# Kernel optimization log

Hardware: AMD Instinct MI355X
Metric: run time of the kernel (lower is better)

Reference implementation:

```python
import jax, jax.numpy as jnp
import numpy as np

B, S, H, D = 4, 2048, 16, 64
DM = H * D  # model dim 1024


def _rope_sincos(seq_len, d2):
    # sin/cos tables for the rotated sub-dimension d2 (= head_dim // 2)
    inv_freq = 1.0 / (10000.0 ** (jnp.arange(0, d2, 2, dtype=jnp.float32) / d2))
    ang = jnp.arange(seq_len, dtype=jnp.float32)[:, None] * inv_freq[None, :]  # (S, d2/2)
    emb = jnp.concatenate([ang, ang], axis=-1)  # (S, d2)
    return jnp.sin(emb), jnp.cos(emb)


def _apply_rope(x, sin, cos):
    # x: (B, S, H, D). Only the first half of head_dim is rotated (faithful to
    # apply_rotary_pos_emb: split -> rotate x1 -> concat with untouched x2).
    x1, x2 = jnp.split(x, 2, axis=-1)  # each (B, S, H, D//2)
    a, b = jnp.split(x1, 2, axis=-1)
    rot = jnp.concatenate([-b, a], axis=-1)  # rotate_half(x1)
    sin = sin[None, :, None, :]
    cos = cos[None, :, None, :]
    return jnp.concatenate([x1 * cos + rot * sin, x2], axis=-1)


def setup_inputs() -> dict:
    key = jax.random.key(0)
    k1, k2 = jax.random.split(key)
    x = jax.random.normal(k1, (B, S, DM), dtype=jnp.float32)
    w_qkv = jax.random.normal(k2, (DM, 3 * H * D), dtype=jnp.float32) / np.sqrt(DM).astype(np.float32)
    mask = jnp.tril(jnp.ones((1, 1, S, S), dtype=bool))  # causal
    return {"x": x, "w_qkv": w_qkv, "mask": mask}


def reference(x, w_qkv, mask):
    b, s, _ = x.shape
    qkv = x @ w_qkv  # (B, S, 3*H*D) fused QKV projection (no bias)
    q, k, v = jnp.split(qkv, 3, axis=-1)
    q = q.reshape(b, s, H, D)
    k = k.reshape(b, s, H, D)
    v = v.reshape(b, s, H, D)
    sin, cos = _rope_sincos(s, D // 2)
    q = _apply_rope(q, sin, cos)
    k = _apply_rope(k, sin, cos)
    # full (B, H, S, S) score matrix, scaled by sqrt(head_dim)
    attn = jnp.einsum('bqhd,bkhd->bhqk', q, k) / jnp.sqrt(jnp.float32(D))
    attn = jnp.where(mask, attn, -jnp.inf)
    attn = jax.nn.softmax(attn, axis=-1)
    out = jnp.einsum('bhqk,bkhd->bqhd', attn, v)
    return out.reshape(b, s, H * D)
```

## Files before the change

### kernel.cpp

```cpp
#include <hip/hip_runtime.h>
#include <hip/hip_bf16.h>

#define SEQ 2048
#define DM 1024
#define NOUT 3072

typedef __attribute__((ext_vector_type(8))) short bf16x8;
typedef __attribute__((ext_vector_type(4))) float f32x4;
typedef __attribute__((ext_vector_type(16))) float f32x16;
typedef __attribute__((ext_vector_type(4))) unsigned int u32x4;

__device__ inline unsigned short bfb(float f) {
    __hip_bfloat16 h = __float2bfloat16(f);
    return __builtin_bit_cast(unsigned short, h);
}

__device__ inline unsigned pk2(float lo, float hi) {
    return (unsigned)bfb(lo) | ((unsigned)bfb(hi) << 16);
}

__device__ inline void gload_lds16(const void* g, void* l) {
    __builtin_amdgcn_global_load_lds(
        (const __attribute__((address_space(1))) unsigned int*)g,
        (__attribute__((address_space(3))) unsigned int*)l, 16, 0, 0);
}

#define M3(a, b, c) fmaxf(fmaxf((a), (b)), (c))

__global__ __launch_bounds__(256) void prep_kernel(
    const float* __restrict__ x, __hip_bfloat16* __restrict__ xb,
    const float* __restrict__ w, __hip_bfloat16* __restrict__ wT,
    float* __restrict__ sintab, float* __restrict__ costab) {
    __shared__ float t[64][65];
    const int b = blockIdx.x, tid = threadIdx.x;
    if (b < 8192) {
        int i = b * 256 + tid;
        float4 v = ((const float4*)x)[i];
        ushort4 o;
        o.x = bfb(v.x); o.y = bfb(v.y); o.z = bfb(v.z); o.w = bfb(v.w);
        ((ushort4*)xb)[i] = o;
    } else if (b < 8960) {
        const int idx = b - 8192;
        const int k0 = (idx & 15) * 64;
        const int n0 = (idx >> 4) * 64;
        for (int i = tid; i < 4096; i += 256) {
            int r = i >> 6, c = i & 63;
            t[r][c] = w[(size_t)(k0 + r) * NOUT + n0 + c];
        }
        __syncthreads();
        for (int i = tid; i < 4096; i += 256) {
            int nl = i >> 6, kl = i & 63;
            wT[(size_t)(n0 + nl) * DM + k0 + kl] = __float2bfloat16(t[kl][nl]);
        }
    } else {
        int i = (b - 8960) * 256 + tid;
        int f = i & 15, s = i >> 4;
        float inv = powf(10000.0f, -(float)f * (1.0f / 16.0f));
        float ang = (float)s * inv;
        sintab[i] = sinf(ang);
        costab[i] = cosf(ang);
    }
}

#define BM 128
#define BN 128
#define BK 32

__global__ __launch_bounds__(256) void qkv_gemm_kernel(
    const __hip_bfloat16* __restrict__ xb, const __hip_bfloat16* __restrict__ wT,
    const float* __restrict__ costab, const float* __restrict__ sintab,
    __hip_bfloat16* __restrict__ Qg, __hip_bfloat16* __restrict__ Kg,
    __hip_bfloat16* __restrict__ Vt) {
    __shared__ __hip_bfloat16 As[BM * BK];
    __shared__ __hip_bfloat16 Bs[BN * BK];
    const int tid = threadIdx.x, lane = tid & 63, wid = tid >> 6;
    const int wm = wid >> 1, wn = wid & 1;
    const int m0 = blockIdx.x * BM, n0 = blockIdx.y * BN;
    const int g = lane >> 4;

    f32x4 acc[4][4] = {};

    for (int k0 = 0; k0 < DM; k0 += BK) {
        __syncthreads();
#pragma unroll
        for (int c2 = 0; c2 < 2; ++c2) {
            const int chunk = wid * 2 + c2;
            gload_lds16(xb + (size_t)(m0 + chunk * 16 + (lane >> 2)) * DM + k0 + (lane & 3) * 8,
                        &As[chunk * 512]);
            gload_lds16(wT + (size_t)(n0 + chunk * 16 + (lane >> 2)) * DM + k0 + (lane & 3) * 8,
                        &Bs[chunk * 512]);
        }
        __syncthreads();
        bf16x8 a[4], b[4];
#pragma unroll
        for (int mf = 0; mf < 4; ++mf)
            a[mf] = *(const bf16x8*)&As[(wm * 64 + mf * 16 + (lane & 15)) * BK + (g << 3)];
#pragma unroll
        for (int nf = 0; nf < 4; ++nf)
            b[nf] = *(const bf16x8*)&Bs[(wn * 64 + nf * 16 + (lane & 15)) * BK + (g << 3)];
#pragma unroll
        for (int mf = 0; mf < 4; ++mf)
#pragma unroll
            for (int nf = 0; nf < 4; ++nf)
                acc[mf][nf] = __builtin_amdgcn_mfma_f32_16x16x32_bf16(a[mf], b[nf], acc[mf][nf], 0, 0, 0);
    }

    const int colbase = n0 + wn * 64;
    const int part = colbase >> 10;
    const int h = (colbase & 1023) >> 6;
    const int d0 = lane & 15;
    const int rowg0 = m0 + wm * 64 + (g << 2);

    if (part == 2) {
#pragma unroll
        for (int mf = 0; mf < 4; ++mf) {
            const int rbase = rowg0 + mf * 16;
            const int b = rbase >> 11, s = rbase & 2047;
            const size_t vb = (size_t)(b * 16 + h) * 64 * SEQ;
#pragma unroll
            for (int nf = 0; nf < 4; ++nf) {
                const int d = nf * 16 + d0;
                ushort4 pk;
                pk.x = bfb(acc[mf][nf][0]);
                pk.y = bfb(acc[mf][nf][1]);
                pk.z = bfb(acc[mf][nf][2]);
                pk.w = bfb(acc[mf][nf][3]);
                *(ushort4*)((unsigned short*)Vt + vb + (size_t)d * SEQ + s) = pk;
            }
        }
    } else {
        __hip_bfloat16* __restrict__ dstT = part ? Kg : Qg;
        const float sc = part ? 1.0f : 0.125f * 1.44269504088896340736f;
#pragma unroll
        for (int mf = 0; mf < 4; ++mf) {
#pragma unroll
            for (int j = 0; j < 4; ++j) {
                const int mg = rowg0 + mf * 16 + j;
                const int b = mg >> 11, s = mg & 2047;
                const float cv = costab[s * 16 + d0];
                const float sv = sintab[s * 16 + d0];
                const float v0 = acc[mf][0][j], v1 = acc[mf][1][j];
                __hip_bfloat16* dst = dstT + ((size_t)(b * 16 + h) * SEQ + s) * 64;
                dst[d0]      = __float2bfloat16((v0 * cv - v1 * sv) * sc);
                dst[16 + d0] = __float2bfloat16((v1 * cv + v0 * sv) * sc);
                dst[32 + d0] = __float2bfloat16(acc[mf][2][j] * sc);
                dst[48 + d0] = __float2bfloat16(acc[mf][3][j] * sc);
            }
        }
    }
}

__global__ __launch_bounds__(256) void attn_fwd_kernel(
    const __hip_bfloat16* __restrict__ Qg, const __hip_bfloat16* __restrict__ Kg,
    const __hip_bfloat16* __restrict__ Vt, float* __restrict__ out) {
    __shared__ __align__(16) char smem[2][16384];
    const int tid = threadIdx.x, lane = tid & 63, wid = tid >> 6;
    const int qt = 15 - (blockIdx.x >> 6);
    const int bh = blockIdx.x & 63;
    const size_t base = (size_t)bh << 17;
    const int ql = lane & 31, hi = lane >> 5;
    const int qb = (qt << 7) + (wid << 5);
    const int qrow = qb + ql;
    const int nkt = 2 * qt + 2;
    const unsigned short* Kgu = (const unsigned short*)Kg + base;
    const unsigned short* Vtu = (const unsigned short*)Vt + base;
    const int b = bh >> 4, h = bh & 15;
    const int lo16 = lane << 4;

    bf16x8 qfrag[4];
    {
        const unsigned short* qp = (const unsigned short*)Qg + base + (size_t)qrow * 64 + hi * 8;
#pragma unroll
        for (int c = 0; c < 4; ++c) qfrag[c] = *(const bf16x8*)(qp + c * 16);
    }

    f32x16 accO[2] = {};
    float m = -INFINITY, l = 0.0f;

    const unsigned short* stsrc;
    int stdst;
    if (wid < 2) {
        stsrc = Kgu + (size_t)(wid * 32 + ql) * 64 + hi * 8;
        stdst = wid * 4096;
    } else {
        stsrc = Vtu + (size_t)((wid - 2) * 32 + ql) * SEQ + hi * 8;
        stdst = 8192 + (wid - 2) * 4096;
    }

    {
#pragma unroll
        for (int c = 0; c < 4; ++c)
            gload_lds16(stsrc + c * 16, &smem[0][stdst + c * 1024]);
    }

    int cur = 0;
#pragma unroll 1
    for (int kt = 0; kt < nkt; ++kt) {
        const int k0 = kt << 6;
        if (kt + 1 < nkt) {
            const int kn = (kt + 1) << 6;
            const unsigned short* sn = (wid < 2) ? stsrc + (size_t)kn * 64 : stsrc + kn;
            char* nb = &smem[cur ^ 1][stdst];
#pragma unroll
            for (int c = 0; c < 4; ++c)
                gload_lds16(sn + c * 16, nb + c * 1024);
            asm volatile("s_waitcnt vmcnt(4)" ::: "memory");
        } else {
            asm volatile("s_waitcnt vmcnt(0)" ::: "memory");
        }
        __builtin_amdgcn_s_barrier();
        __builtin_amdgcn_sched_barrier(0);

        if (k0 <= qb + 31) {
            const char* Ks = smem[cur];
            const char* Vs = smem[cur] + 8192;

            f32x16 st[2] = {};
            __builtin_amdgcn_s_setprio(1);
#pragma unroll
            for (int c = 0; c < 4; ++c) {
                bf16x8 kf0 = *(const bf16x8*)(Ks + c * 1024 + lo16);
                bf16x8 kf1 = *(const bf16x8*)(Ks + 4096 + c * 1024 + lo16);
                st[0] = __builtin_amdgcn_mfma_f32_32x32x16_bf16(kf0, qfrag[c], st[0], 0, 0, 0);
                st[1] = __builtin_amdgcn_mfma_f32_32x32x16_bf16(kf1, qfrag[c], st[1], 0, 0, 0);
            }
            __builtin_amdgcn_s_setprio(0);

            if (k0 + 63 > qb) {
#pragma unroll
                for (int t = 0; t < 2; ++t)
#pragma unroll
                    for (int r = 0; r < 16; ++r) {
                        const int kg = k0 + 32 * t + (r & 3) + 8 * (r >> 2) + 4 * hi;
                        if (kg > qrow) st[t][r] = -INFINITY;
                    }
            }

            float x0 = M3(st[0][0], st[0][1], st[0][2]);
            float x1 = M3(st[0][3], st[0][4], st[0][5]);
            float x2 = M3(st[0][6], st[0][7], st[0][8]);
            float x3 = M3(st[0][9], st[0][10], st[0][11]);
            float x4 = M3(st[0][12], st[0][13], st[0][14]);
            float x5 = M3(st[0][15], st[1][0], st[1][1]);
            float x6 = M3(st[1][2], st[1][3], st[1][4]);
            float x7 = M3(st[1][5], st[1][6], st[1][7]);
            float x8 = M3(st[1][8], st[1][9], st[1][10]);
            float x9 = M3(st[1][11], st[1][12], st[1][13]);
            float xa = fmaxf(st[1][14], st[1][15]);
            float y0 = M3(x0, x1, x2), y1 = M3(x3, x4, x5);
            float y2 = M3(x6, x7, x8), y3 = M3(x9, xa, y0);
            float tm = M3(y1, y2, y3);
            tm = fmaxf(tm, __shfl_xor(tm, 32, 64));

            if (__any(tm > m + 8.0f)) {
                const float mn = fmaxf(m, tm);
                const float scl = __builtin_amdgcn_exp2f(m - mn);
                m = mn;
                l *= scl;
#pragma unroll
                for (int db = 0; db < 2; ++db)
#pragma unroll
                    for (int r = 0; r < 16; ++r) accO[db][r] *= scl;
            }

            float s0 = 0.0f, s1 = 0.0f, s2 = 0.0f, s3 = 0.0f;
#pragma unroll
            for (int r = 0; r < 16; r += 4) {
                float p00 = __builtin_amdgcn_exp2f(st[0][r + 0] - m);
                float p01 = __builtin_amdgcn_exp2f(st[0][r + 1] - m);
                float p02 = __builtin_amdgcn_exp2f(st[0][r + 2] - m);
                float p03 = __builtin_amdgcn_exp2f(st[0][r + 3] - m);
                float p10 = __builtin_amdgcn_exp2f(st[1][r + 0] - m);
                float p11 = __builtin_amdgcn_exp2f(st[1][r + 1] - m);
                float p12 = __builtin_amdgcn_exp2f(st[1][r + 2] - m);
                float p13 = __builtin_amdgcn_exp2f(st[1][r + 3] - m);
                st[0][r + 0] = p00; st[0][r + 1] = p01; st[0][r + 2] = p02; st[0][r + 3] = p03;
                st[1][r + 0] = p10; st[1][r + 1] = p11; st[1][r + 2] = p12; st[1][r + 3] = p13;
                s0 += p00 + p01; s1 += p02 + p03;
                s2 += p10 + p11; s3 += p12 + p13;
            }
            float ls = (s0 + s1) + (s2 + s3);
            ls += __shfl_xor(ls, 32, 64);
            l += ls;

            bf16x8 pfrag[4];
#pragma unroll
            for (int ks = 0; ks < 4; ++ks) {
                const int t = ks >> 1, rb = (ks & 1) * 8;
                unsigned a0 = pk2(st[t][rb + 0], st[t][rb + 1]);
                unsigned a1 = pk2(st[t][rb + 2], st[t][rb + 3]);
                unsigned b0 = pk2(st[t][rb + 4], st[t][rb + 5]);
                unsigned b1 = pk2(st[t][rb + 6], st[t][rb + 7]);
                asm("v_permlane32_swap_b32 %0, %1" : "+v"(a0), "+v"(b0));
                asm("v_permlane32_swap_b32 %0, %1" : "+v"(a1), "+v"(b1));
                u32x4 w;
                w[0] = a0;
                w[1] = a1;
                w[2] = b0;
                w[3] = b1;
                pfrag[ks] = __builtin_bit_cast(bf16x8, w);
            }

            __builtin_amdgcn_s_setprio(1);
#pragma unroll
            for (int ks = 0; ks < 4; ++ks) {
#pragma unroll
                for (int db = 0; db < 2; ++db) {
                    bf16x8 vf = *(const bf16x8*)(Vs + (db * 4 + ks) * 1024 + lo16);
                    accO[db] = __builtin_amdgcn_mfma_f32_32x32x16_bf16(vf, pfrag[ks], accO[db], 0, 0, 0);
                }
            }
            __builtin_amdgcn_s_setprio(0);
        }

        __builtin_amdgcn_sched_barrier(0);
        __builtin_amdgcn_s_barrier();
        cur ^= 1;
    }

    const float invl = 1.0f / l;
    float* orow = out + (size_t)(b * SEQ + qrow) * DM + h * 64;
#pragma unroll
    for (int db = 0; db < 2; ++db)
#pragma unroll
        for (int rg = 0; rg < 4; ++rg) {
            float4 v;
            v.x = accO[db][rg * 4 + 0] * invl;
            v.y = accO[db][rg * 4 + 1] * invl;
            v.z = accO[db][rg * 4 + 2] * invl;
            v.w = accO[db][rg * 4 + 3] * invl;
            *(float4*)(orow + db * 32 + rg * 8 + hi * 4) = v;
        }
}

extern "C" void kernel_launch(void* const* d_in, const int* in_sizes, int n_in,
                              void* d_out, int out_size, void* d_ws, size_t ws_size,
                              hipStream_t stream) {
    const float* x = (const float*)d_in[0];
    const float* w = (const float*)d_in[1];
    float* out = (float*)d_out;
    char* ws = (char*)d_ws;

    __hip_bfloat16* xb  = (__hip_bfloat16*)(ws + 0);
    __hip_bfloat16* wT  = (__hip_bfloat16*)(ws + 16777216);
    __hip_bfloat16* Qg  = (__hip_bfloat16*)(ws + 23068672);
    __hip_bfloat16* Kg  = (__hip_bfloat16*)(ws + 39845888);
    __hip_bfloat16* Vt  = (__hip_bfloat16*)(ws + 56623104);
    float* costab       = (float*)(ws + 73400320);
    float* sintab       = (float*)(ws + 73531392);

    prep_kernel<<<dim3(9088), dim3(256), 0, stream>>>(x, xb, w, wT, sintab, costab);
    qkv_gemm_kernel<<<dim3(64, 24), dim3(256), 0, stream>>>(xb, wT, costab, sintab, Qg, Kg, Vt);
    attn_fwd_kernel<<<dim3(1024), dim3(256), 0, stream>>>(Qg, Kg, Vt, out);
}
```

Measured before the change: 142.6 us.

## Enlarge QKV GEMM tiles to 256x256 with double-buffered LDS prefetch

Rewrites the QKV projection GEMM to use 512-thread blocks computing 256x256 output tiles with a K step of 64. A 128KB dynamic LDS buffer is double-buffered so the next K slab is loaded while MFMAs run on the current one. MFMA sections are wrapped in raised wave priority. Each wave now holds 8x4 accumulator fragments, which raises operand reuse and cuts per-tile sync overhead. In exchange, the grid shrinks to 384 blocks with about one block per CU, which may cause tail imbalance, and register pressure rises.

```diff
diff --git a/kernel.cpp b/kernel.cpp
--- a/kernel.cpp
+++ b/kernel.cpp
@@ -62,58 +62,86 @@
     }
 }
 
-#define BM 128
-#define BN 128
-#define BK 32
-
-__global__ __launch_bounds__(256) void qkv_gemm_kernel(
+__device__ __forceinline__ void qkv_tile(const char* Ab, const char* Bb, f32x4 (&acc)[8][4]) {
+#pragma unroll
+    for (int ks = 0; ks < 2; ++ks) {
+        bf16x8 a[8], b[4];
+#pragma unroll
+        for (int mf = 0; mf < 8; ++mf) a[mf] = *(const bf16x8*)(Ab + mf * 2048 + ks * 1024);
+#pragma unroll
+        for (int nf = 0; nf < 4; ++nf) b[nf] = *(const bf16x8*)(Bb + nf * 2048 + ks * 1024);
+        __builtin_amdgcn_s_setprio(1);
+#pragma unroll
+        for (int mf = 0; mf < 8; ++mf)
+#pragma unroll
+            for (int nf = 0; nf < 4; ++nf)
+                acc[mf][nf] = __builtin_amdgcn_mfma_f32_16x16x32_bf16(a[mf], b[nf], acc[mf][nf], 0, 0, 0);
+        __builtin_amdgcn_s_setprio(0);
+    }
+}
+
+__global__ __launch_bounds__(512, 2) void qkv_gemm_kernel(
     const __hip_bfloat16* __restrict__ xb, const __hip_bfloat16* __restrict__ wT,
     const float* __restrict__ costab, const float* __restrict__ sintab,
     __hip_bfloat16* __restrict__ Qg, __hip_bfloat16* __restrict__ Kg,
     __hip_bfloat16* __restrict__ Vt) {
-    __shared__ __hip_bfloat16 As[BM * BK];
-    __shared__ __hip_bfloat16 Bs[BN * BK];
+    extern __shared__ __align__(16) char smc[];
     const int tid = threadIdx.x, lane = tid & 63, wid = tid >> 6;
-    const int wm = wid >> 1, wn = wid & 1;
-    const int m0 = blockIdx.x * BM, n0 = blockIdx.y * BN;
-    const int g = lane >> 4;
-
-    f32x4 acc[4][4] = {};
-
-    for (int k0 = 0; k0 < DM; k0 += BK) {
+    const int wm = wid >> 2, wn = wid & 3;
+    const int m0 = blockIdx.x * 256, n0 = blockIdx.y * 256;
+
+    const int row_lane = lane >> 2;
+    const int k_lane = (lane & 3) * 8;
+    const __hip_bfloat16* sA0 = xb + (size_t)(m0 +       wid * 16 + row_lane) * DM + k_lane;
+    const __hip_bfloat16* sA1 = xb + (size_t)(m0 + 128 + wid * 16 + row_lane) * DM + k_lane;
+    const __hip_bfloat16* sB0 = wT + (size_t)(n0 +       wid * 16 + row_lane) * DM + k_lane;
+    const __hip_bfloat16* sB1 = wT + (size_t)(n0 + 128 + wid * 16 + row_lane) * DM + k_lane;
+    const int dA0 = wid * 2048, dA1 = 16384 + wid * 2048;
+    const int dB0 = 32768 + wid * 2048, dB1 = 49152 + wid * 2048;
+
+    const int fragoff = (lane & 15) * 64 + (lane >> 4) * 16;
+    const char* Abase = smc + wm * 16384 + fragoff;
+    const char* Bbase = smc + 32768 + (wn >> 1) * 16384 + (wn & 1) * 8192 + fragoff;
+
+    f32x4 acc[8][4] = {};
+
+#pragma unroll
+    for (int s = 0; s < 2; ++s) {
+        gload_lds16(sA0 + s * 32, smc + dA0 + s * 1024);
+        gload_lds16(sA1 + s * 32, smc + dA1 + s * 1024);
+        gload_lds16(sB0 + s * 32, smc + dB0 + s * 1024);
+        gload_lds16(sB1 + s * 32, smc + dB1 + s * 1024);
+    }
+    __syncthreads();
+
+#pragma unroll 1
+    for (int t = 0; t < 15; ++t) {
+        const int kk = (t + 1) * 64;
+        const int nb = ((t + 1) & 1) * 65536;
+#pragma unroll
+        for (int s = 0; s < 2; ++s) {
+            gload_lds16(sA0 + kk + s * 32, smc + nb + dA0 + s * 1024);
+            gload_lds16(sA1 + kk + s * 32, smc + nb + dA1 + s * 1024);
+            gload_lds16(sB0 + kk + s * 32, smc + nb + dB0 + s * 1024);
+            gload_lds16(sB1 + kk + s * 32, smc + nb + dB1 + s * 1024);
+        }
+        __builtin_amdgcn_sched_barrier(0);
+        const int cb = (t & 1) * 65536;
+        qkv_tile(Abase + cb, Bbase + cb, acc);
         __syncthreads();
-#pragma unroll
-        for (int c2 = 0; c2 < 2; ++c2) {
-            const int chunk = wid * 2 + c2;
-            gload_lds16(xb + (size_t)(m0 + chunk * 16 + (lane >> 2)) * DM + k0 + (lane & 3) * 8,
-                        &As[chunk * 512]);
-            gload_lds16(wT + (size_t)(n0 + chunk * 16 + (lane >> 2)) * DM + k0 + (lane & 3) * 8,
-                        &Bs[chunk * 512]);
-        }
-        __syncthreads();
-        bf16x8 a[4], b[4];
-#pragma unroll
-        for (int mf = 0; mf < 4; ++mf)
-            a[mf] = *(const bf16x8*)&As[(wm * 64 + mf * 16 + (lane & 15)) * BK + (g << 3)];
-#pragma unroll
-        for (int nf = 0; nf < 4; ++nf)
-            b[nf] = *(const bf16x8*)&Bs[(wn * 64 + nf * 16 + (lane & 15)) * BK + (g << 3)];
-#pragma unroll
-        for (int mf = 0; mf < 4; ++mf)
-#pragma unroll
-            for (int nf = 0; nf < 4; ++nf)
-                acc[mf][nf] = __builtin_amdgcn_mfma_f32_16x16x32_bf16(a[mf], b[nf], acc[mf][nf], 0, 0, 0);
-    }
+    }
+    qkv_tile(Abase + 65536, Bbase + 65536, acc);
 
     const int colbase = n0 + wn * 64;
     const int part = colbase >> 10;
     const int h = (colbase & 1023) >> 6;
     const int d0 = lane & 15;
-    const int rowg0 = m0 + wm * 64 + (g << 2);
+    const int g = lane >> 4;
+    const int rowg0 = m0 + wm * 128 + (g << 2);
 
     if (part == 2) {
 #pragma unroll
-        for (int mf = 0; mf < 4; ++mf) {
+        for (int mf = 0; mf < 8; ++mf) {
             const int rbase = rowg0 + mf * 16;
             const int b = rbase >> 11, s = rbase & 2047;
             const size_t vb = (size_t)(b * 16 + h) * 64 * SEQ;
@@ -132,7 +160,7 @@
         __hip_bfloat16* __restrict__ dstT = part ? Kg : Qg;
         const float sc = part ? 1.0f : 0.125f * 1.44269504088896340736f;
 #pragma unroll
-        for (int mf = 0; mf < 4; ++mf) {
+        for (int mf = 0; mf < 8; ++mf) {
 #pragma unroll
             for (int j = 0; j < 4; ++j) {
                 const int mg = rowg0 + mf * 16 + j;
@@ -349,7 +377,14 @@
     float* costab       = (float*)(ws + 73400320);
     float* sintab       = (float*)(ws + 73531392);
 
+    static bool qkv_attr_set = false;
+    if (!qkv_attr_set) {
+        hipFuncSetAttribute((const void*)qkv_gemm_kernel,
+                            hipFuncAttributeMaxDynamicSharedMemorySize, 131072);
+        qkv_attr_set = true;
+    }
+
     prep_kernel<<<dim3(9088), dim3(256), 0, stream>>>(x, xb, w, wT, sintab, costab);
-    qkv_gemm_kernel<<<dim3(64, 24), dim3(256), 0, stream>>>(xb, wT, costab, sintab, Qg, Kg, Vt);
+    qkv_gemm_kernel<<<dim3(32, 12), dim3(512), 131072, stream>>>(xb, wT, costab, sintab, Qg, Kg, Vt);
     attn_fwd_kernel<<<dim3(1024), dim3(256), 0, stream>>>(Qg, Kg, Vt, out);
 }
```

Result: slower. 148.5 us (+4.1%).

## Double-buffer QKV GEMM with larger 256x128 tiles and 512 threads

Applied to the files above, without the earlier changes.

Rewrites the QKV projection GEMM to use 256x128 block tiles with 8 waves, BK=64, and a double-buffered dynamic LDS pipeline. Loads for the next k-step are issued before computing the current one, with vmcnt-based waits and s_setprio around the MFMA bursts. The aim is to hide global-to-LDS latency and halve the number of barriers per unit of work. In exchange it uses 96KB of LDS and one block per CU, which lowers occupancy, and it halves the grid size.

```diff
diff --git a/kernel.cpp b/kernel.cpp
--- a/kernel.cpp
+++ b/kernel.cpp
@@ -62,53 +62,80 @@
     }
 }
 
-#define BM 128
-#define BN 128
-#define BK 32
-
-__global__ __launch_bounds__(256) void qkv_gemm_kernel(
+#define PERBUF 49152
+
+__device__ __forceinline__ void qkv_tile(const char* Ab, const char* Bb, f32x4 (&acc)[4][4]) {
+#pragma unroll
+    for (int ks = 0; ks < 2; ++ks) {
+        bf16x8 a[4], b[4];
+#pragma unroll
+        for (int mf = 0; mf < 4; ++mf) a[mf] = *(const bf16x8*)(Ab + mf * 2048 + ks * 1024);
+#pragma unroll
+        for (int nf = 0; nf < 4; ++nf) b[nf] = *(const bf16x8*)(Bb + nf * 2048 + ks * 1024);
+        __builtin_amdgcn_s_setprio(1);
+#pragma unroll
+        for (int mf = 0; mf < 4; ++mf)
+#pragma unroll
+            for (int nf = 0; nf < 4; ++nf)
+                acc[mf][nf] = __builtin_amdgcn_mfma_f32_16x16x32_bf16(a[mf], b[nf], acc[mf][nf], 0, 0, 0);
+        __builtin_amdgcn_s_setprio(0);
+    }
+}
+
+__global__ __launch_bounds__(512, 1) void qkv_gemm_kernel(
     const __hip_bfloat16* __restrict__ xb, const __hip_bfloat16* __restrict__ wT,
     const float* __restrict__ costab, const float* __restrict__ sintab,
     __hip_bfloat16* __restrict__ Qg, __hip_bfloat16* __restrict__ Kg,
     __hip_bfloat16* __restrict__ Vt) {
-    __shared__ __hip_bfloat16 As[BM * BK];
-    __shared__ __hip_bfloat16 Bs[BN * BK];
+    extern __shared__ __align__(16) char smc[];
     const int tid = threadIdx.x, lane = tid & 63, wid = tid >> 6;
     const int wm = wid >> 1, wn = wid & 1;
-    const int m0 = blockIdx.x * BM, n0 = blockIdx.y * BN;
-    const int g = lane >> 4;
+    const int m0 = blockIdx.x * 256, n0 = blockIdx.y * 128;
+    const int rl = lane & 15;
+    const int kl = (lane >> 4) * 8;
+
+    const __hip_bfloat16* sA = xb + (size_t)(m0 + wid * 32 + rl) * DM + kl;
+    const __hip_bfloat16* sB = wT + (size_t)(n0 + wid * 16 + rl) * DM + kl;
+
+#define QKV_STAGE(kk, bufoff)                                                           \
+    do {                                                                                \
+        _Pragma("unroll")                                                               \
+        for (int s = 0; s < 4; ++s)                                                     \
+            gload_lds16(sA + (size_t)(s >> 1) * (16 * DM) + (kk) + (s & 1) * 32,        \
+                        smc + (bufoff) + wid * 4096 + (s >> 1) * 2048 + (s & 1) * 1024);\
+        _Pragma("unroll")                                                               \
+        for (int s = 0; s < 2; ++s)                                                     \
+            gload_lds16(sB + (kk) + s * 32,                                             \
+                        smc + (bufoff) + 32768 + wid * 2048 + s * 1024);                \
+    } while (0)
 
     f32x4 acc[4][4] = {};
-
-    for (int k0 = 0; k0 < DM; k0 += BK) {
-        __syncthreads();
-#pragma unroll
-        for (int c2 = 0; c2 < 2; ++c2) {
-            const int chunk = wid * 2 + c2;
-            gload_lds16(xb + (size_t)(m0 + chunk * 16 + (lane >> 2)) * DM + k0 + (lane & 3) * 8,
-                        &As[chunk * 512]);
-            gload_lds16(wT + (size_t)(n0 + chunk * 16 + (lane >> 2)) * DM + k0 + (lane & 3) * 8,
-                        &Bs[chunk * 512]);
-        }
-        __syncthreads();
-        bf16x8 a[4], b[4];
-#pragma unroll
-        for (int mf = 0; mf < 4; ++mf)
-            a[mf] = *(const bf16x8*)&As[(wm * 64 + mf * 16 + (lane & 15)) * BK + (g << 3)];
-#pragma unroll
-        for (int nf = 0; nf < 4; ++nf)
-            b[nf] = *(const bf16x8*)&Bs[(wn * 64 + nf * 16 + (lane & 15)) * BK + (g << 3)];
-#pragma unroll
-        for (int mf = 0; mf < 4; ++mf)
-#pragma unroll
-            for (int nf = 0; nf < 4; ++nf)
-                acc[mf][nf] = __builtin_amdgcn_mfma_f32_16x16x32_bf16(a[mf], b[nf], acc[mf][nf], 0, 0, 0);
-    }
+    const int Aoff = wm * 8192 + lane * 16;
+    const int Boff = 32768 + wn * 8192 + lane * 16;
+
+    QKV_STAGE(0, 0);
+
+#pragma unroll 1
+    for (int t = 0; t < 15; ++t) {
+        const int kk = (t + 1) * 64;
+        QKV_STAGE(kk, ((t + 1) & 1) * PERBUF);
+        asm volatile("s_waitcnt vmcnt(6)" ::: "memory");
+        __builtin_amdgcn_s_barrier();
+        __builtin_amdgcn_sched_barrier(0);
+        const int cb = (t & 1) * PERBUF;
+        qkv_tile(smc + cb + Aoff, smc + cb + Boff, acc);
+        __builtin_amdgcn_sched_barrier(0);
+        __builtin_amdgcn_s_barrier();
+    }
+    asm volatile("s_waitcnt vmcnt(0)" ::: "memory");
+    __builtin_amdgcn_s_barrier();
+    qkv_tile(smc + PERBUF + Aoff, smc + PERBUF + Boff, acc);
 
     const int colbase = n0 + wn * 64;
     const int part = colbase >> 10;
     const int h = (colbase & 1023) >> 6;
     const int d0 = lane & 15;
+    const int g = lane >> 4;
     const int rowg0 = m0 + wm * 64 + (g << 2);
 
     if (part == 2) {
@@ -349,7 +376,14 @@
     float* costab       = (float*)(ws + 73400320);
     float* sintab       = (float*)(ws + 73531392);
 
+    static bool qkv_attr_set = false;
+    if (!qkv_attr_set) {
+        hipFuncSetAttribute((const void*)qkv_gemm_kernel,
+                            hipFuncAttributeMaxDynamicSharedMemorySize, 98304);
+        qkv_attr_set = true;
+    }
+
     prep_kernel<<<dim3(9088), dim3(256), 0, stream>>>(x, xb, w, wT, sintab, costab);
-    qkv_gemm_kernel<<<dim3(64, 24), dim3(256), 0, stream>>>(xb, wT, costab, sintab, Qg, Kg, Vt);
+    qkv_gemm_kernel<<<dim3(32, 24), dim3(512), 98304, stream>>>(xb, wT, costab, sintab, Qg, Kg, Vt);
     attn_fwd_kernel<<<dim3(1024), dim3(256), 0, stream>>>(Qg, Kg, Vt, out);
 }
```

After: 157.2 us. 1.1x slower.

## Load K/V fragments directly from global memory, dropping LDS staging and barriers

Applied to the files above, without the earlier changes.

The attention kernel no longer stages K and V tiles into double-buffered shared memory via global_load_lds with block-wide barriers. Each wave now reads its K and V MFMA fragments straight from global memory and runs only its own causal trip count (per-wave nkt). This removes LDS traffic, barriers and the idle iterations of waves already past the diagonal. The cost is that all four waves re-read the same K/V from global memory or L2 without any software prefetch, so load latency is exposed on every iteration.

```diff
diff --git a/kernel.cpp b/kernel.cpp
--- a/kernel.cpp
+++ b/kernel.cpp
@@ -153,7 +153,6 @@
 __global__ __launch_bounds__(256) void attn_fwd_kernel(
     const __hip_bfloat16* __restrict__ Qg, const __hip_bfloat16* __restrict__ Kg,
     const __hip_bfloat16* __restrict__ Vt, float* __restrict__ out) {
-    __shared__ __align__(16) char smem[2][16384];
     const int tid = threadIdx.x, lane = tid & 63, wid = tid >> 6;
     const int qt = 15 - (blockIdx.x >> 6);
     const int bh = blockIdx.x & 63;
@@ -161,11 +160,10 @@
     const int ql = lane & 31, hi = lane >> 5;
     const int qb = (qt << 7) + (wid << 5);
     const int qrow = qb + ql;
-    const int nkt = 2 * qt + 2;
-    const unsigned short* Kgu = (const unsigned short*)Kg + base;
-    const unsigned short* Vtu = (const unsigned short*)Vt + base;
     const int b = bh >> 4, h = bh & 15;
-    const int lo16 = lane << 4;
+
+    const unsigned short* kp = (const unsigned short*)Kg + base + (size_t)ql * 64 + hi * 8;
+    const unsigned short* vp = (const unsigned short*)Vt + base + (size_t)ql * SEQ + hi * 8;
 
     bf16x8 qfrag[4];
     {
@@ -177,145 +175,115 @@
     f32x16 accO[2] = {};
     float m = -INFINITY, l = 0.0f;
 
-    const unsigned short* stsrc;
-    int stdst;
-    if (wid < 2) {
-        stsrc = Kgu + (size_t)(wid * 32 + ql) * 64 + hi * 8;
-        stdst = wid * 4096;
-    } else {
-        stsrc = Vtu + (size_t)((wid - 2) * 32 + ql) * SEQ + hi * 8;
-        stdst = 8192 + (wid - 2) * 4096;
-    }
-
-    {
-#pragma unroll
-        for (int c = 0; c < 4; ++c)
-            gload_lds16(stsrc + c * 16, &smem[0][stdst + c * 1024]);
-    }
-
-    int cur = 0;
+    const int nkt = ((qb + 31) >> 6) + 1;
+
 #pragma unroll 1
     for (int kt = 0; kt < nkt; ++kt) {
         const int k0 = kt << 6;
-        if (kt + 1 < nkt) {
-            const int kn = (kt + 1) << 6;
-            const unsigned short* sn = (wid < 2) ? stsrc + (size_t)kn * 64 : stsrc + kn;
-            char* nb = &smem[cur ^ 1][stdst];
-#pragma unroll
-            for (int c = 0; c < 4; ++c)
-                gload_lds16(sn + c * 16, nb + c * 1024);
-            asm volatile("s_waitcnt vmcnt(4)" ::: "memory");
-        } else {
-            asm volatile("s_waitcnt vmcnt(0)" ::: "memory");
-        }
-        __builtin_amdgcn_s_barrier();
-        __builtin_amdgcn_sched_barrier(0);
-
-        if (k0 <= qb + 31) {
-            const char* Ks = smem[cur];
-            const char* Vs = smem[cur] + 8192;
-
-            f32x16 st[2] = {};
-            __builtin_amdgcn_s_setprio(1);
-#pragma unroll
-            for (int c = 0; c < 4; ++c) {
-                bf16x8 kf0 = *(const bf16x8*)(Ks + c * 1024 + lo16);
-                bf16x8 kf1 = *(const bf16x8*)(Ks + 4096 + c * 1024 + lo16);
-                st[0] = __builtin_amdgcn_mfma_f32_32x32x16_bf16(kf0, qfrag[c], st[0], 0, 0, 0);
-                st[1] = __builtin_amdgcn_mfma_f32_32x32x16_bf16(kf1, qfrag[c], st[1], 0, 0, 0);
-            }
-            __builtin_amdgcn_s_setprio(0);
-
-            if (k0 + 63 > qb) {
-#pragma unroll
-                for (int t = 0; t < 2; ++t)
-#pragma unroll
-                    for (int r = 0; r < 16; ++r) {
-                        const int kg = k0 + 32 * t + (r & 3) + 8 * (r >> 2) + 4 * hi;
-                        if (kg > qrow) st[t][r] = -INFINITY;
-                    }
-            }
-
-            float x0 = M3(st[0][0], st[0][1], st[0][2]);
-            float x1 = M3(st[0][3], st[0][4], st[0][5]);
-            float x2 = M3(st[0][6], st[0][7], st[0][8]);
-            float x3 = M3(st[0][9], st[0][10], st[0][11]);
-            float x4 = M3(st[0][12], st[0][13], st[0][14]);
-            float x5 = M3(st[0][15], st[1][0], st[1][1]);
-            float x6 = M3(st[1][2], st[1][3], st[1][4]);
-            float x7 = M3(st[1][5], st[1][6], st[1][7]);
-            float x8 = M3(st[1][8], st[1][9], st[1][10]);
-            float x9 = M3(st[1][11], st[1][12], st[1][13]);
-            float xa = fmaxf(st[1][14], st[1][15]);
-            float y0 = M3(x0, x1, x2), y1 = M3(x3, x4, x5);
-            float y2 = M3(x6, x7, x8), y3 = M3(x9, xa, y0);
-            float tm = M3(y1, y2, y3);
-            tm = fmaxf(tm, __shfl_xor(tm, 32, 64));
-
-            if (__any(tm > m + 8.0f)) {
-                const float mn = fmaxf(m, tm);
-                const float scl = __builtin_amdgcn_exp2f(m - mn);
-                m = mn;
-                l *= scl;
-#pragma unroll
-                for (int db = 0; db < 2; ++db)
-#pragma unroll
-                    for (int r = 0; r < 16; ++r) accO[db][r] *= scl;
-            }
-
-            float s0 = 0.0f, s1 = 0.0f, s2 = 0.0f, s3 = 0.0f;
-#pragma unroll
-            for (int r = 0; r < 16; r += 4) {
-                float p00 = __builtin_amdgcn_exp2f(st[0][r + 0] - m);
-                float p01 = __builtin_amdgcn_exp2f(st[0][r + 1] - m);
-                float p02 = __builtin_amdgcn_exp2f(st[0][r + 2] - m);
-                float p03 = __builtin_amdgcn_exp2f(st[0][r + 3] - m);
-                float p10 = __builtin_amdgcn_exp2f(st[1][r + 0] - m);
-                float p11 = __builtin_amdgcn_exp2f(st[1][r + 1] - m);
-                float p12 = __builtin_amdgcn_exp2f(st[1][r + 2] - m);
-                float p13 = __builtin_amdgcn_exp2f(st[1][r + 3] - m);
-                st[0][r + 0] = p00; st[0][r + 1] = p01; st[0][r + 2] = p02; st[0][r + 3] = p03;
-                st[1][r + 0] = p10; st[1][r + 1] = p11; st[1][r + 2] = p12; st[1][r + 3] = p13;
-                s0 += p00 + p01; s1 += p02 + p03;
-                s2 += p10 + p11; s3 += p12 + p13;
-            }
-            float ls = (s0 + s1) + (s2 + s3);
-            ls += __shfl_xor(ls, 32, 64);
-            l += ls;
-
-            bf16x8 pfrag[4];
-#pragma unroll
-            for (int ks = 0; ks < 4; ++ks) {
-                const int t = ks >> 1, rb = (ks & 1) * 8;
-                unsigned a0 = pk2(st[t][rb + 0], st[t][rb + 1]);
-                unsigned a1 = pk2(st[t][rb + 2], st[t][rb + 3]);
-                unsigned b0 = pk2(st[t][rb + 4], st[t][rb + 5]);
-                unsigned b1 = pk2(st[t][rb + 6], st[t][rb + 7]);
-                asm("v_permlane32_swap_b32 %0, %1" : "+v"(a0), "+v"(b0));
-                asm("v_permlane32_swap_b32 %0, %1" : "+v"(a1), "+v"(b1));
-                u32x4 w;
-                w[0] = a0;
-                w[1] = a1;
-                w[2] = b0;
-                w[3] = b1;
-                pfrag[ks] = __builtin_bit_cast(bf16x8, w);
-            }
-
-            __builtin_amdgcn_s_setprio(1);
-#pragma unroll
-            for (int ks = 0; ks < 4; ++ks) {
-#pragma unroll
-                for (int db = 0; db < 2; ++db) {
-                    bf16x8 vf = *(const bf16x8*)(Vs + (db * 4 + ks) * 1024 + lo16);
-                    accO[db] = __builtin_amdgcn_mfma_f32_32x32x16_bf16(vf, pfrag[ks], accO[db], 0, 0, 0);
+        const unsigned short* kpt = kp + (size_t)k0 * 64;
+        const unsigned short* vpt = vp + k0;
+
+        f32x16 st[2] = {};
+        __builtin_amdgcn_s_setprio(1);
+#pragma unroll
+        for (int c = 0; c < 4; ++c) {
+            bf16x8 kf0 = *(const bf16x8*)(kpt + c * 16);
+            bf16x8 kf1 = *(const bf16x8*)(kpt + 2048 + c * 16);
+            st[0] = __builtin_amdgcn_mfma_f32_32x32x16_bf16(kf0, qfrag[c], st[0], 0, 0, 0);
+            st[1] = __builtin_amdgcn_mfma_f32_32x32x16_bf16(kf1, qfrag[c], st[1], 0, 0, 0);
+        }
+        __builtin_amdgcn_s_setprio(0);
+
+        bf16x8 vf[2][4];
+#pragma unroll
+        for (int db = 0; db < 2; ++db)
+#pragma unroll
+            for (int ks = 0; ks < 4; ++ks)
+                vf[db][ks] = *(const bf16x8*)(vpt + (size_t)db * 32 * SEQ + ks * 16);
+
+        if (k0 + 63 > qb) {
+#pragma unroll
+            for (int t = 0; t < 2; ++t)
+#pragma unroll
+                for (int r = 0; r < 16; ++r) {
+                    const int kg = k0 + 32 * t + (r & 3) + 8 * (r >> 2) + 4 * hi;
+                    if (kg > qrow) st[t][r] = -INFINITY;
                 }
-            }
-            __builtin_amdgcn_s_setprio(0);
-        }
-
-        __builtin_amdgcn_sched_barrier(0);
-        __builtin_amdgcn_s_barrier();
-        cur ^= 1;
+        }
+
+        float x0 = M3(st[0][0], st[0][1], st[0][2]);
+        float x1 = M3(st[0][3], st[0][4], st[0][5]);
+        float x2 = M3(st[0][6], st[0][7], st[0][8]);
+        float x3 = M3(st[0][9], st[0][10], st[0][11]);
+        float x4 = M3(st[0][12], st[0][13], st[0][14]);
+        float x5 = M3(st[0][15], st[1][0], st[1][1]);
+        float x6 = M3(st[1][2], st[1][3], st[1][4]);
+        float x7 = M3(st[1][5], st[1][6], st[1][7]);
+        float x8 = M3(st[1][8], st[1][9], st[1][10]);
+        float x9 = M3(st[1][11], st[1][12], st[1][13]);
+        float xa = fmaxf(st[1][14], st[1][15]);
+        float y0 = M3(x0, x1, x2), y1 = M3(x3, x4, x5);
+        float y2 = M3(x6, x7, x8), y3 = M3(x9, xa, y0);
+        float tm = M3(y1, y2, y3);
+        tm = fmaxf(tm, __shfl_xor(tm, 32, 64));
+
+        if (__any(tm > m + 8.0f)) {
+            const float mn = fmaxf(m, tm);
+            const float scl = __builtin_amdgcn_exp2f(m - mn);
+            m = mn;
+            l *= scl;
+#pragma unroll
+            for (int db = 0; db < 2; ++db)
+#pragma unroll
+                for (int r = 0; r < 16; ++r) accO[db][r] *= scl;
+        }
+
+        float s0 = 0.0f, s1 = 0.0f, s2 = 0.0f, s3 = 0.0f;
+#pragma unroll
+        for (int r = 0; r < 16; r += 4) {
+            float p00 = __builtin_amdgcn_exp2f(st[0][r + 0] - m);
+            float p01 = __builtin_amdgcn_exp2f(st[0][r + 1] - m);
+            float p02 = __builtin_amdgcn_exp2f(st[0][r + 2] - m);
+            float p03 = __builtin_amdgcn_exp2f(st[0][r + 3] - m);
+            float p10 = __builtin_amdgcn_exp2f(st[1][r + 0] - m);
+            float p11 = __builtin_amdgcn_exp2f(st[1][r + 1] - m);
+            float p12 = __builtin_amdgcn_exp2f(st[1][r + 2] - m);
+            float p13 = __builtin_amdgcn_exp2f(st[1][r + 3] - m);
+            st[0][r + 0] = p00; st[0][r + 1] = p01; st[0][r + 2] = p02; st[0][r + 3] = p03;
+            st[1][r + 0] = p10; st[1][r + 1] = p11; st[1][r + 2] = p12; st[1][r + 3] = p13;
+            s0 += p00 + p01; s1 += p02 + p03;
+            s2 += p10 + p11; s3 += p12 + p13;
+        }
+        float ls = (s0 + s1) + (s2 + s3);
+        ls += __shfl_xor(ls, 32, 64);
+        l += ls;
+
+        bf16x8 pfrag[4];
+#pragma unroll
+        for (int ks = 0; ks < 4; ++ks) {
+            const int t = ks >> 1, rb = (ks & 1) * 8;
+            unsigned a0 = pk2(st[t][rb + 0], st[t][rb + 1]);
+            unsigned a1 = pk2(st[t][rb + 2], st[t][rb + 3]);
+            unsigned b0 = pk2(st[t][rb + 4], st[t][rb + 5]);
+            unsigned b1 = pk2(st[t][rb + 6], st[t][rb + 7]);
+            asm("v_permlane32_swap_b32 %0, %1" : "+v"(a0), "+v"(b0));
+            asm("v_permlane32_swap_b32 %0, %1" : "+v"(a1), "+v"(b1));
+            u32x4 w;
+            w[0] = a0;
+            w[1] = a1;
+            w[2] = b0;
+            w[3] = b1;
+            pfrag[ks] = __builtin_bit_cast(bf16x8, w);
+        }
+
+        __builtin_amdgcn_s_setprio(1);
+#pragma unroll
+        for (int ks = 0; ks < 4; ++ks) {
+#pragma unroll
+            for (int db = 0; db < 2; ++db)
+                accO[db] = __builtin_amdgcn_mfma_f32_32x32x16_bf16(vf[db][ks], pfrag[ks], accO[db], 0, 0, 0);
+        }
+        __builtin_amdgcn_s_setprio(0);
     }
 
     const float invl = 1.0f / l;
```

Measured after the change: 201.2 us. +41.1%, slower.
